# Performance work log

Measured on AMD Instinct MI355X. Metric: run time of the kernel, lower is better.

## Reference

```python
import jax, jax.numpy as jnp
import numpy as np

B, S, E, H, T = 32, 4096, 256, 256, 64  # bsz, seq_len, enc_dim, lstm_hid, turns/sample


def setup_inputs() -> dict:
    key = jax.random.key(0)
    k1, k2, k3, k4, k5, k6, k7 = jax.random.split(key, 7)
    encoder_output = jax.random.normal(k1, (B, S, E), dtype=jnp.float32)
    # equal-length turn structure: even partition of [0, S) into T non-empty segments
    ends = (jnp.arange(1, T + 1, dtype=jnp.int32) * S) // T - 1  # [T], strictly increasing
    his_turn_end_ids = jnp.broadcast_to(ends, (B, T))
    s = 1.0 / np.sqrt(H)
    W_ih = jax.random.uniform(k2, (4 * H, E), minval=-s, maxval=s, dtype=jnp.float32)
    W_hh = jax.random.uniform(k3, (4 * H, H), minval=-s, maxval=s, dtype=jnp.float32)
    b_ih = jax.random.uniform(k4, (4 * H,), minval=-s, maxval=s, dtype=jnp.float32)
    b_hh = jax.random.uniform(k5, (4 * H,), minval=-s, maxval=s, dtype=jnp.float32)
    sf = 1.0 / np.sqrt(H + E)
    fc_w = jax.random.uniform(k6, (1, H + E), minval=-sf, maxval=sf, dtype=jnp.float32)
    fc_b = jax.random.uniform(k7, (1,), minval=-sf, maxval=sf, dtype=jnp.float32)
    return {"encoder_output": encoder_output, "his_turn_end_ids": his_turn_end_ids,
            "W_ih": W_ih, "W_hh": W_hh, "b_ih": b_ih, "b_hh": b_hh,
            "fc_w": fc_w, "fc_b": fc_b}


def _lstm_cell(x, h, c, W_ih, W_hh, b):
    g = x @ W_ih.T + h @ W_hh.T + b          # [N, 4H], torch gate order i,f,g,o
    i, f, gg, o = jnp.split(g, 4, axis=-1)
    c = jax.nn.sigmoid(f) * c + jax.nn.sigmoid(i) * jnp.tanh(gg)
    h = jax.nn.sigmoid(o) * jnp.tanh(c)
    return h, c


def reference(encoder_output, his_turn_end_ids, W_ih, W_hh, b_ih, b_hh, fc_w, fc_b):
    Bc, Sc, Ec = encoder_output.shape
    Tc = his_turn_end_ids.shape[1]
    ends = his_turn_end_ids.astype(jnp.int32)
    starts = jnp.concatenate([jnp.zeros((Bc, 1), jnp.int32), ends[:, :-1] + 1], axis=1)
    # segment mean via exclusive prefix sum: sum[s:e+1] = csum[e+1] - csum[s]
    csum = jnp.concatenate([jnp.zeros((Bc, 1, Ec), encoder_output.dtype),
                            jnp.cumsum(encoder_output, axis=1)], axis=1)  # [B, S+1, E]
    seg_sum = (jnp.take_along_axis(csum, (ends + 1)[..., None], axis=1)
               - jnp.take_along_axis(csum, starts[..., None], axis=1))   # [B, T, E]
    lens = (ends - starts + 1).astype(encoder_output.dtype)
    states = seg_sum / lens[..., None]                                   # his_turn_states

    # length-2 LSTM over (state_j, state_{j+1}) for each anchor j in [0, T-3]
    J = Tc - 2
    x1 = states[:, :J].reshape(-1, Ec)       # [B*J, E]
    x2 = states[:, 1:J + 1].reshape(-1, Ec)
    b = b_ih + b_hh
    h0 = jnp.zeros((x1.shape[0], W_hh.shape[1]), states.dtype)
    h1, c1 = _lstm_cell(x1, h0, h0, W_ih, W_hh, b)
    h2, _ = _lstm_cell(x2, h1, c1, W_ih, W_hh, b)
    src_last = h2.reshape(Bc, J, -1)         # [B, J, H]

    # logit(i,j,k) = fc([src_last[i,j]; states[i, j+2+k]]) for k < T-2-j
    Wh, We = fc_w[0, :src_last.shape[-1]], fc_w[0, src_last.shape[-1]:]
    a = src_last @ Wh                        # [B, J]
    t = states @ We                          # [B, T]
    jdx = jnp.arange(J)
    kdx = jnp.arange(J)
    tgt_idx = jdx[:, None] + 2 + kdx[None, :]        # [J, J]
    valid = tgt_idx < Tc
    tgt_idx = jnp.clip(tgt_idx, 0, Tc - 1)
    logits = a[:, :, None] + t[:, tgt_idx] + fc_b[0]  # [B, J, J]
    neg_inf = jnp.asarray(-1e30, logits.dtype)
    masked = jnp.where(valid[None], logits, neg_inf)
    # CE with target class 0 (first candidate, the true next turn)
    loss = jax.nn.logsumexp(masked, axis=-1) - logits[..., 0]  # [B, J]
    return jnp.mean(loss)


if __name__ == "__main__":
    out = reference(**setup_inputs())
    print(out)
```

## Files before the change

### kernel.cpp

```cpp
#include <hip/hip_runtime.h>
#include <math.h>

#define B 32
#define S 4096
#define E 256
#define H 256
#define T 64
#define J (T - 2)
#define NROWS (B * S)

__device__ __forceinline__ float dot4(float4 v, float4 w) {
    return fmaf(v.x, w.x, fmaf(v.y, w.y, fmaf(v.z, w.z, v.w * w.w)));
}

__global__ __launch_bounds__(256) void row_dot4_kernel(
    const float* __restrict__ enc,
    const float* __restrict__ We,
    float* __restrict__ d) {
    const int tid  = threadIdx.x;
    const int lane = tid & 63;
    const int wv   = (blockIdx.x << 2) | (tid >> 6);

    const float4  w4 = reinterpret_cast<const float4*>(We)[lane];
    const float4* p  = reinterpret_cast<const float4*>(enc)
                     + (size_t)wv * 256 + lane;
    float s0 = dot4(p[0],   w4);
    float s1 = dot4(p[64],  w4);
    float s2 = dot4(p[128], w4);
    float s3 = dot4(p[192], w4);
#pragma unroll
    for (int off = 32; off >= 1; off >>= 1) {
        s0 += __shfl_xor(s0, off, 64);
        s1 += __shfl_xor(s1, off, 64);
        s2 += __shfl_xor(s2, off, 64);
        s3 += __shfl_xor(s3, off, 64);
    }
    if (lane == 0)
        reinterpret_cast<float4*>(d)[wv] = make_float4(s0, s1, s2, s3);
}

__global__ __launch_bounds__(64) void seg_mean_kernel(
    const float* __restrict__ d,
    const int* __restrict__ ends,
    float* __restrict__ t) {
    const int g    = blockIdx.x;
    const int lane = threadIdx.x;
    const int tau  = g & (T - 1);
    const int b    = g >> 6;

    const int e  = ends[g];
    const int st = (tau == 0) ? 0 : (ends[g - 1] + 1);

    const float* db = d + (size_t)b * S;
    float s = 0.0f;
    for (int i = st + lane; i <= e; i += 64) s += db[i];

#pragma unroll
    for (int off = 32; off >= 1; off >>= 1)
        s += __shfl_xor(s, off, 64);

    if (lane == 0) t[g] = s / (float)(e - st + 1);
}

__global__ __launch_bounds__(64) void lse_kernel(
    const float* __restrict__ t,
    float* __restrict__ out) {
    const int lane = threadIdx.x;
    __shared__ float tl[B * T];

    const float4* tp = reinterpret_cast<const float4*>(t);
#pragma unroll
    for (int k = 0; k < 8; ++k) {
        float4 v = tp[lane + k * 64];
        const int i = 4 * (lane + k * 64);
        tl[i] = v.x; tl[i + 1] = v.y; tl[i + 2] = v.z; tl[i + 3] = v.w;
    }
    __syncthreads();

    float ls = 0.0f;
    if (lane < B) {
        const float* tb = tl + lane * T;
        float M = tb[T - 1], a = 1.0f;
        for (int j = J - 1; j >= 0; --j) {
            ls += logf(a) + M - tb[j + 2];
            if (j > 0) {
                const float x  = tb[j + 1];
                const float M2 = fmaxf(M, x);
                a = a * __expf(M - M2) + __expf(x - M2);
                M = M2;
            }
        }
    }

#pragma unroll
    for (int off = 32; off >= 1; off >>= 1)
        ls += __shfl_xor(ls, off, 64);
    if (lane == 0) out[0] = ls / (float)(B * J);
}

extern "C" void kernel_launch(void* const* d_in, const int* in_sizes, int n_in,
                              void* d_out, int out_size, void* d_ws, size_t ws_size,
                              hipStream_t stream) {
    const float* enc  = (const float*)d_in[0];
    const int*   ends = (const int*)d_in[1];
    const float* We   = (const float*)d_in[6] + H;

    float* d   = (float*)d_ws;
    float* t   = d + NROWS;
    float* out = (float*)d_out;

    row_dot4_kernel<<<NROWS / 16, 256, 0, stream>>>(enc, We, d);
    seg_mean_kernel<<<B * T, 64, 0, stream>>>(d, ends, t);
    lse_kernel<<<1, 64, 0, stream>>>(t, out);
}
```

Baseline: 35.75 us.

## Fuse segment-mean and logsumexp tail into one per-batch kernel with atomic finish

Merges the segment-mean and logsumexp kernels into a single kernel with one block per batch. Each block computes its segment means into shared memory, runs the loss recurrence, and atomically adds its partial loss. A last-block counter then writes the final mean. This removes one kernel launch and the intermediate t buffer, but the tail now runs on only 32 blocks and the accumulator reset depends on the first kernel running before it.

```diff
diff --git a/kernel.cpp b/kernel.cpp
--- a/kernel.cpp
+++ b/kernel.cpp
@@ -16,10 +16,14 @@
 __global__ __launch_bounds__(256) void row_dot4_kernel(
     const float* __restrict__ enc,
     const float* __restrict__ We,
-    float* __restrict__ d) {
+    float* __restrict__ d,
+    float* __restrict__ accum,
+    unsigned int* __restrict__ counter) {
     const int tid  = threadIdx.x;
     const int lane = tid & 63;
     const int wv   = (blockIdx.x << 2) | (tid >> 6);
+
+    if (blockIdx.x == 0 && tid == 0) { *accum = 0.0f; *counter = 0u; }
 
     const float4  w4 = reinterpret_cast<const float4*>(We)[lane];
     const float4* p  = reinterpret_cast<const float4*>(enc)
@@ -39,63 +43,68 @@
         reinterpret_cast<float4*>(d)[wv] = make_float4(s0, s1, s2, s3);
 }
 
-__global__ __launch_bounds__(64) void seg_mean_kernel(
+__global__ __launch_bounds__(256) void batch_tail_kernel(
     const float* __restrict__ d,
     const int* __restrict__ ends,
-    float* __restrict__ t) {
-    const int g    = blockIdx.x;
-    const int lane = threadIdx.x;
-    const int tau  = g & (T - 1);
-    const int b    = g >> 6;
+    float* __restrict__ accum,
+    unsigned int* __restrict__ counter,
+    float* __restrict__ out) {
+    const int b    = blockIdx.x;
+    const int tid  = threadIdx.x;
+    const int w    = tid >> 6;
+    const int lane = tid & 63;
 
-    const int e  = ends[g];
-    const int st = (tau == 0) ? 0 : (ends[g - 1] + 1);
+    __shared__ int   el[T];
+    __shared__ float tt[T];
+
+    if (tid < T) el[tid] = ends[b * T + tid];
+    __syncthreads();
 
     const float* db = d + (size_t)b * S;
-    float s = 0.0f;
-    for (int i = st + lane; i <= e; i += 64) s += db[i];
-
+    float v[16];
+    int   st[16], e[16];
 #pragma unroll
-    for (int off = 32; off >= 1; off >>= 1)
-        s += __shfl_xor(s, off, 64);
-
-    if (lane == 0) t[g] = s / (float)(e - st + 1);
-}
-
-__global__ __launch_bounds__(64) void lse_kernel(
-    const float* __restrict__ t,
-    float* __restrict__ out) {
-    const int lane = threadIdx.x;
-    __shared__ float tl[B * T];
-
-    const float4* tp = reinterpret_cast<const float4*>(t);
+    for (int k = 0; k < 16; ++k) {
+        const int seg = w * 16 + k;
+        e[k]  = el[seg];
+        st[k] = (seg == 0) ? 0 : (el[seg - 1] + 1);
+        const int i = st[k] + lane;
+        v[k] = (i <= e[k]) ? db[i] : 0.0f;
+    }
 #pragma unroll
-    for (int k = 0; k < 8; ++k) {
-        float4 v = tp[lane + k * 64];
-        const int i = 4 * (lane + k * 64);
-        tl[i] = v.x; tl[i + 1] = v.y; tl[i + 2] = v.z; tl[i + 3] = v.w;
+    for (int k = 0; k < 16; ++k)
+        for (int i = st[k] + 64 + lane; i <= e[k]; i += 64) v[k] += db[i];
+#pragma unroll
+    for (int k = 0; k < 16; ++k) {
+#pragma unroll
+        for (int off = 32; off >= 1; off >>= 1)
+            v[k] += __shfl_xor(v[k], off, 64);
+        if (lane == 0)
+            tt[w * 16 + k] = v[k] / (float)(e[k] - st[k] + 1);
     }
     __syncthreads();
 
-    float ls = 0.0f;
-    if (lane < B) {
-        const float* tb = tl + lane * T;
-        float M = tb[T - 1], a = 1.0f;
+    if (tid == 0) {
+        float M = tt[T - 1], a = 1.0f, ls = 0.0f;
         for (int j = J - 1; j >= 0; --j) {
-            ls += logf(a) + M - tb[j + 2];
+            ls += logf(a) + M - tt[j + 2];
             if (j > 0) {
-                const float x  = tb[j + 1];
+                const float x  = tt[j + 1];
                 const float M2 = fmaxf(M, x);
                 a = a * __expf(M - M2) + __expf(x - M2);
                 M = M2;
             }
         }
+        atomicAdd(accum, ls);
+        __threadfence();
+        const unsigned int old = atomicAdd(counter, 1u);
+        if (old == B - 1) {
+            __threadfence();
+            const float tot = __hip_atomic_load(accum, __ATOMIC_ACQUIRE,
+                                                __HIP_MEMORY_SCOPE_AGENT);
+            out[0] = tot / (float)(B * J);
+        }
     }
-
-#pragma unroll
-    for (int off = 32; off >= 1; off >>= 1)
-        ls += __shfl_xor(ls, off, 64);
-    if (lane == 0) out[0] = ls / (float)(B * J);
 }
 
 extern "C" void kernel_launch(void* const* d_in, const int* in_sizes, int n_in,
@@ -105,11 +114,11 @@
     const int*   ends = (const int*)d_in[1];
     const float* We   = (const float*)d_in[6] + H;
 
-    float* d   = (float*)d_ws;
-    float* t   = d + NROWS;
-    float* out = (float*)d_out;
+    float*        dbuf    = (float*)d_ws;
+    float*        accum   = dbuf + NROWS;
+    unsigned int* counter = (unsigned int*)(accum + 1);
+    float*        out     = (float*)d_out;
 
-    row_dot4_kernel<<<NROWS / 16, 256, 0, stream>>>(enc, We, d);
-    seg_mean_kernel<<<B * T, 64, 0, stream>>>(d, ends, t);
-    lse_kernel<<<1, 64, 0, stream>>>(t, out);
+    row_dot4_kernel<<<NROWS / 16, 256, 0, stream>>>(enc, We, dbuf, accum, counter);
+    batch_tail_kernel<<<B, 256, 0, stream>>>(dbuf, ends, accum, counter, out);
 }
```

After: 41.29 us. 1.15x slower.
